# Performance work log

Measured on AMD Instinct MI355X. Metric: run time of the kernel, lower is better.

Reference implementation:

```python
import jax, jax.numpy as jnp
import numpy as np
from math import comb

LEVEL = 16
LENGTH = 64
TOPK = 2
SIZE = 512
BATCH = 32
NEG = -1e8


def _catalan(n_leaves):
    # number of distinct binary trees over n_leaves leaves
    m = n_leaves - 1
    return comb(2 * m, m) // (m + 1)


def _offsets(length, level):
    # cell offset of each chart level: level l occupies (length - l) cells
    return np.cumsum([0] + [length - l for l in range(level)])


def setup_inputs() -> dict:
    key = jax.random.key(0)
    K, B, size, level, length = TOPK, BATCH, SIZE, LEVEL, LENGTH
    L, N = length - level, level
    off = _offsets(length, level)
    ncells = int(off[-1])
    ks = jax.random.split(key, 5)
    chart_h = jax.random.normal(ks[0], (K, B, ncells, size), jnp.float32)
    chart_s = jax.random.normal(ks[1], (K, B, ncells, 1), jnp.float32)
    mat = jax.random.normal(ks[2], (size, size), jnp.float32) / np.sqrt(size).astype(np.float32)
    Wc = jax.random.normal(ks[3], (2 * size, size), jnp.float32) / np.sqrt(2 * size).astype(np.float32)
    bc = jnp.zeros((size,), jnp.float32)
    # structural gather indices: left child = (level n, pos), right child = (level level-1-n, pos+n+1)
    l_idx = np.zeros((L, N), np.int64)
    r_idx = np.zeros((L, N), np.int64)
    for pos in range(L):
        for n in range(N):
            l_idx[pos, n] = off[n] + pos
            r_idx[pos, n] = off[level - 1 - n] + pos + n + 1
    return {
        'chart_h': chart_h, 'chart_s': chart_s,
        'l_index': jnp.asarray(l_idx.reshape(-1)), 'r_index': jnp.asarray(r_idx.reshape(-1)),
        'mat': mat, 'Wc': Wc, 'bc': bc,
    }


def _penalty_mask(level, N, K):
    # Faithful to penalize_incomplete_splits: idx = i // K**2 == 0 for i < K*K,
    # so only the n_idx==0 block is ever penalized. l_level=0, r_level=level-1.
    M = N * K * K
    mask = np.zeros(M, bool)
    for i in range(K * K):
        lk, rk = i // K, i % K
        if _catalan(0 + 1) < lk + 1 or _catalan((level - 1) + 1) < rk + 1:
            mask[i] = True
    return jnp.asarray(mask)


def reference(chart_h, chart_s, l_index, r_index, mat, Wc, bc):
    K, B, ncells, size = chart_h.shape
    level = LEVEL
    N = level
    L = l_index.shape[0] // N
    M = N * K * K
    # gather child states from charts: (K,B,L,N,size) -> (B,L,N,K,size)
    lh = jnp.moveaxis(chart_h[:, :, l_index].reshape(K, B, L, N, size), 0, 3)
    rh = jnp.moveaxis(chart_h[:, :, r_index].reshape(K, B, L, N, size), 0, 3)
    ls = jnp.moveaxis(chart_s[:, :, l_index].reshape(K, B, L, N), 0, 3)  # (B,L,N,K)
    rs = jnp.moveaxis(chart_s[:, :, r_index].reshape(K, B, L, N), 0, 3)
    # bilinear composition score: (B,L,N,K_l,K_r)
    s_raw = jnp.einsum('blnkd,de,blnje->blnkj', lh, mat, rh)
    # flat combo index = n*K*K + lk*K + rk; add child scores
    s = (s_raw + ls[..., :, None] + rs[..., None, :]).reshape(B, L, M)
    s = jnp.where(_penalty_mask(level, N, K), jnp.float32(NEG), s)
    topk_s, topk_idx = jax.lax.top_k(s, K)  # (B,L,K), sorted descending like torch.topk
    # dense compose over all N*K*K combos
    combo_lh = jnp.repeat(lh, K, axis=3).reshape(B, L, M, size)   # lk = z // K
    combo_rh = jnp.tile(rh, (1, 1, 1, K, 1)).reshape(B, L, M, size)  # rk = z % K
    all_h = jnp.tanh(jnp.concatenate([combo_lh, combo_rh], axis=-1) @ Wc + bc)
    topk_h = jnp.take_along_axis(all_h, topk_idx[..., None], axis=2)  # (B,L,K,size)
    # UnitNorm normalize_func
    topk_h = topk_h / jnp.linalg.norm(topk_h, axis=-1, keepdims=True)
    topk_s = topk_s[..., None]  # (B,L,K,1) to match torch shape
    if _catalan(N + 1) < K:  # static no-op at this level
        topk_s = topk_s.at[:, :, _catalan(N + 1):].set(NEG)
    topk_n_idx = topk_idx // (K * K)
    topk_lk = (topk_idx % (K * K)) // K
    topk_rk = (topk_idx % (K * K)) % K
    return topk_h, topk_s, topk_n_idx, topk_lk, topk_rk
```

## Files before the change

kernel.cpp:

```cpp
#include <hip/hip_runtime.h>
#include <cstdint>
#include <cstddef>

#define B_DIM   32
#define L_DIM   48
#define NCELLS  904
#define SZ      512
#define NEGF    (-1e8f)
#define DELTA   0.25f
#define MAXC    32

#define OFF_S   1572864
#define OFF_N   1575936
#define OFF_L   1579008
#define OFF_R   1582080

typedef _Float16  f16x8 __attribute__((ext_vector_type(8)));
typedef float     f32x4 __attribute__((ext_vector_type(4)));

static __device__ __forceinline__ uint16_t f2bf(float f) {
    uint32_t u = __builtin_bit_cast(uint32_t, f);
    u += 0x7fffu + ((u >> 16) & 1u);
    return (uint16_t)(u >> 16);
}

#define GLD16(gp, lp) __builtin_amdgcn_global_load_lds(                        \
        (__attribute__((address_space(1))) void*)(gp),                         \
        (__attribute__((address_space(3))) void*)(lp), 16, 0, 0)

static __device__ __forceinline__ int level_off(int n) {
    return n * 64 - (n * (n - 1)) / 2;
}

__global__ __launch_bounds__(256)
void prep_mat(const float* __restrict__ mat, _Float16* __restrict__ mat16)
{
    const size_t j = ((size_t)blockIdx.x * 256 + threadIdx.x) * 8;
    const float4 c = *(const float4*)(mat + j);
    const float4 d = *(const float4*)(mat + j + 4);
    f16x8 w;
    w[0]=(_Float16)(c.x*64.f); w[1]=(_Float16)(c.y*64.f);
    w[2]=(_Float16)(c.z*64.f); w[3]=(_Float16)(c.w*64.f);
    w[4]=(_Float16)(d.x*64.f); w[5]=(_Float16)(d.y*64.f);
    w[6]=(_Float16)(d.z*64.f); w[7]=(_Float16)(d.w*64.f);
    *(f16x8*)(mat16 + j) = w;
}

__global__ __launch_bounds__(256, 3)
void gemm_fused(const float* __restrict__ A,
                const _Float16* __restrict__ Bm,
                _Float16* __restrict__ C)
{
    __shared__ float    As32[64 * 32];
    __shared__ _Float16 Bs[256 * 32];

    const int t = threadIdx.x;
    const int wave = t >> 6, lane = t & 63;
    const int n0 = blockIdx.x * 256;
    const int m0 = blockIdx.y * 64;
    const int col_l = lane & 15, quad = lane >> 4;

    f32x4 acc[4][4];
#pragma unroll
    for (int i = 0; i < 4; ++i)
#pragma unroll
        for (int j = 0; j < 4; ++j) acc[i][j] = (f32x4){0.f, 0.f, 0.f, 0.f};

    const int arow = lane >> 3;
    const int aswz = ((lane & 7) ^ arow) * 4;
    const int asw_rd = (col_l & 7) << 4;

    for (int ks = 0; ks < 16; ++ks) {
        const int k0 = ks * 32;
        __syncthreads();
#pragma unroll
        for (int i = 0; i < 2; ++i) {
            const int q = wave * 2 + i;
            GLD16(A + (size_t)(m0 + q * 8 + arow) * 512 + k0 + aswz,
                  (char*)As32 + q * 1024);
        }
#pragma unroll
        for (int i = 0; i < 4; ++i) {
            const int q = wave * 4 + i;
            GLD16(Bm + (size_t)(n0 + q * 16 + col_l) * 512 + k0 + quad * 8,
                  (char*)Bs + q * 1024);
        }
        __syncthreads();

        f16x8 af[4];
#pragma unroll
        for (int mi = 0; mi < 4; ++mi) {
            const char* rb = (const char*)As32 + mi * 2048 + col_l * 128;
            const f32x4 p0 = *(const f32x4*)(rb + ((quad * 32 +  0) ^ asw_rd));
            const f32x4 p1 = *(const f32x4*)(rb + ((quad * 32 + 16) ^ asw_rd));
#pragma unroll
            for (int j = 0; j < 4; ++j) {
                af[mi][j]     = (_Float16)(p0[j] * 16.f);
                af[mi][j + 4] = (_Float16)(p1[j] * 16.f);
            }
        }
#pragma unroll
        for (int ni = 0; ni < 4; ++ni) {
            const f16x8 bf = *(const f16x8*)&Bs[(wave * 4 + ni) * 512 + lane * 8];
#pragma unroll
            for (int mi = 0; mi < 4; ++mi)
                acc[mi][ni] = __builtin_amdgcn_mfma_f32_16x16x32_f16(
                    af[mi], bf, acc[mi][ni], 0, 0, 0);
        }
    }

#pragma unroll
    for (int ni = 0; ni < 4; ++ni) {
        const int ncol = n0 + wave * 64 + ni * 16 + col_l;
#pragma unroll
        for (int mi = 0; mi < 4; ++mi) {
            const int mrow = m0 + mi * 16 + quad * 4;
#pragma unroll
            for (int r = 0; r < 4; ++r)
                C[(size_t)(mrow + r) * 512 + ncol] = (_Float16)acc[mi][ni][r];
        }
    }
}

static __device__ __forceinline__ void emit_outputs(
    int row, int i1, int i2, float v1, float v2, float* out)
{
    out[OFF_S + row * 2 + 0] = v1;
    out[OFF_S + row * 2 + 1] = v2;
    out[OFF_N + row * 2 + 0] = (float)(i1 >> 2);
    out[OFF_N + row * 2 + 1] = (float)(i2 >> 2);
    out[OFF_L + row * 2 + 0] = (float)((i1 >> 1) & 1);
    out[OFF_L + row * 2 + 1] = (float)((i2 >> 1) & 1);
    out[OFF_R + row * 2 + 0] = (float)(i1 & 1);
    out[OFF_R + row * 2 + 1] = (float)(i2 & 1);
}

static __device__ __forceinline__ void gather_x(
    int row, int pos, int b, const int* top_z,
    const float* __restrict__ chart_h, uint16_t* __restrict__ X, int tid)
{
#pragma unroll
    for (int kq = 0; kq < 2; ++kq) {
        const int z = top_z[kq];
        const int n = z >> 2, lk = (z >> 1) & 1, rk = z & 1;
        const int lcell = level_off(n) + pos;
        const int rcell = level_off(15 - n) + pos + n + 1;
        const float* srcl = chart_h + ((size_t)(lk * B_DIM + b) * NCELLS + lcell) * SZ;
        const float* srcr = chart_h + ((size_t)(rk * B_DIM + b) * NCELLS + rcell) * SZ;
        uint16_t* dst = X + ((size_t)row * 2 + kq) * 1024;
        const int e = tid * 2;
        const float2 a = *(const float2*)(srcl + e);
        const float2 c = *(const float2*)(srcr + e);
        *(uint32_t*)(dst + e)       = (uint32_t)f2bf(a.x) | ((uint32_t)f2bf(a.y) << 16);
        *(uint32_t*)(dst + 512 + e) = (uint32_t)f2bf(c.x) | ((uint32_t)f2bf(c.y) << 16);
    }
}

__global__ __launch_bounds__(256)
void score_topk(const float* __restrict__ chart_h,
                const _Float16* __restrict__ T16,
                const float* __restrict__ chart_s,
                uint32_t* __restrict__ items,
                int* __restrict__ rowbase,
                int* __restrict__ counter,
                int* __restrict__ flags,
                uint16_t* __restrict__ X,
                float* __restrict__ out)
{
    const int b   = blockIdx.x / L_DIM;
    const int pos = blockIdx.x % L_DIM;
    const int row = blockIdx.x;
    const int wave = threadIdx.x >> 6, lane = threadIdx.x & 63;

    __shared__ float s_sh[64];
    __shared__ int top_z[2];
    __shared__ int flag_sh;

#pragma unroll
    for (int ni = 0; ni < 4; ++ni) {
        const int n = wave * 4 + ni;
        const int lcell = level_off(n) + pos;
        const int rcell = level_off(15 - n) + pos + n + 1;

        const float* lp0 = chart_h + ((size_t)(0 * B_DIM + b) * NCELLS + lcell) * SZ + lane * 8;
        const float* lp1 = chart_h + ((size_t)(1 * B_DIM + b) * NCELLS + lcell) * SZ + lane * 8;
        const float4 l0a = *(const float4*)lp0, l0b = *(const float4*)(lp0 + 4);
        const float4 l1a = *(const float4*)lp1, l1b = *(const float4*)(lp1 + 4);
        const f16x8 t0 = *(const f16x8*)(T16 + ((size_t)(0 * B_DIM + b) * NCELLS + rcell) * SZ + lane * 8);
        const f16x8 t1 = *(const f16x8*)(T16 + ((size_t)(1 * B_DIM + b) * NCELLS + rcell) * SZ + lane * 8);

        float l0[8] = {l0a.x, l0a.y, l0a.z, l0a.w, l0b.x, l0b.y, l0b.z, l0b.w};
        float l1[8] = {l1a.x, l1a.y, l1a.z, l1a.w, l1b.x, l1b.y, l1b.z, l1b.w};

        float d00 = 0.f, d01 = 0.f, d10 = 0.f, d11 = 0.f;
#pragma unroll
        for (int j = 0; j < 8; ++j) {
            const float c0 = (float)t0[j], c1 = (float)t1[j];
            d00 += l0[j] * c0; d01 += l0[j] * c1;
            d10 += l1[j] * c0; d11 += l1[j] * c1;
        }
#pragma unroll
        for (int o = 32; o > 0; o >>= 1) {
            d00 += __shfl_down(d00, o);
            d01 += __shfl_down(d01, o);
            d10 += __shfl_down(d10, o);
            d11 += __shfl_down(d11, o);
        }
        if (lane == 0) {
            const float ls0 = chart_s[(size_t)(0 * B_DIM + b) * NCELLS + lcell];
            const float ls1 = chart_s[(size_t)(1 * B_DIM + b) * NCELLS + lcell];
            const float rs0 = chart_s[(size_t)(0 * B_DIM + b) * NCELLS + rcell];
            const float rs1 = chart_s[(size_t)(1 * B_DIM + b) * NCELLS + rcell];
            const float inv = 1.0f / 1024.0f;
            s_sh[n * 4 + 0] = d00 * inv + ls0 + rs0;
            s_sh[n * 4 + 1] = d01 * inv + ls0 + rs1;
            s_sh[n * 4 + 2] = d10 * inv + ls1 + rs0;
            s_sh[n * 4 + 3] = d11 * inv + ls1 + rs1;
        }
    }
    __syncthreads();

    if (threadIdx.x < 64) {
        float v = s_sh[lane];
        if (lane == 2 || lane == 3) v = NEGF;
        float v1 = v; int i1 = lane;
#pragma unroll
        for (int o = 32; o > 0; o >>= 1) {
            float ov = __shfl_down(v1, o);
            int   oi = __shfl_down(i1, o);
            if (ov > v1 || (ov == v1 && oi < i1)) { v1 = ov; i1 = oi; }
        }
        v1 = __shfl(v1, 0); i1 = __shfl(i1, 0);
        float v2 = (lane == i1) ? -3.4e38f : v; int i2 = lane;
#pragma unroll
        for (int o = 32; o > 0; o >>= 1) {
            float ov = __shfl_down(v2, o);
            int   oi = __shfl_down(i2, o);
            if (ov > v2 || (ov == v2 && oi < i2)) { v2 = ov; i2 = oi; }
        }
        v2 = __shfl(v2, 0); i2 = __shfl(i2, 0);
        float v3 = (lane == i1 || lane == i2) ? -3.4e38f : v;
#pragma unroll
        for (int o = 32; o > 0; o >>= 1) {
            const float ov = __shfl_down(v3, o);
            if (ov > v3) v3 = ov;
        }
        v3 = __shfl(v3, 0);

        const int f = (v1 - v2 < DELTA) || (v2 - v3 < DELTA);
        const bool cand = (v >= v2 - DELTA);
        const unsigned long long mask = __ballot(cand);
        const int nc_full = __popcll(mask);
        const int nc = nc_full < MAXC ? nc_full : MAXC;
        int base = 0;
        if (lane == 0) {
            flags[row] = f ? nc : 0;
            flag_sh = f;
            if (f) base = atomicAdd(counter, nc);
            rowbase[row] = base;
            top_z[0] = i1; top_z[1] = i2;
            if (!f) emit_outputs(row, i1, i2, v1, v2, out);
        }
        base = __shfl(base, 0);
        if (f && cand) {
            const int rank = __popcll(mask & ((1ull << lane) - 1ull));
            if (rank < MAXC) items[base + rank] = ((uint32_t)row << 6) | (uint32_t)lane;
        }
    }
    __syncthreads();

    if (!flag_sh)
        gather_x(row, pos, b, top_z, chart_h, X, threadIdx.x);
}

__global__ __launch_bounds__(256)
void refine_eval(const float* __restrict__ chart_h,
                 const float* __restrict__ chart_s,
                 const float* __restrict__ mat,
                 const uint32_t* __restrict__ items,
                 const int* __restrict__ counter,
                 float* __restrict__ exval)
{
    const int total = *counter;
    const int t = threadIdx.x;
    const int wave = t >> 6, lane = t & 63;

    __shared__ float lh_sh[2][512];
    __shared__ float psum[2][4];

    for (int p = blockIdx.x; 2 * p < total; p += gridDim.x) {
        const int it0 = 2 * p;
        const int it1v = (2 * p + 1 < total);
        const uint32_t item0 = items[it0];
        const uint32_t item1 = it1v ? items[it0 + 1] : item0;

        int rowA = item0 >> 6, zA = item0 & 63;
        int bA = rowA / L_DIM, posA = rowA % L_DIM;
        int nA = zA >> 2, lkA = (zA >> 1) & 1, rkA = zA & 1;
        int lcA = level_off(nA) + posA, rcA = level_off(15 - nA) + posA + nA + 1;
        int rowB = item1 >> 6, zB = item1 & 63;
        int bB = rowB / L_DIM, posB = rowB % L_DIM;
        int nB = zB >> 2, lkB = (zB >> 1) & 1, rkB = zB & 1;
        int lcB = level_off(nB) + posB, rcB = level_off(15 - nB) + posB + nB + 1;

        const float* lhA = chart_h + ((size_t)(lkA * B_DIM + bA) * NCELLS + lcA) * SZ;
        const float* rhA = chart_h + ((size_t)(rkA * B_DIM + bA) * NCELLS + rcA) * SZ;
        const float* lhB = chart_h + ((size_t)(lkB * B_DIM + bB) * NCELLS + lcB) * SZ;
        const float* rhB = chart_h + ((size_t)(rkB * B_DIM + bB) * NCELLS + rcB) * SZ;

        __syncthreads();
        lh_sh[0][t] = lhA[t]; lh_sh[0][t + 256] = lhA[t + 256];
        lh_sh[1][t] = lhB[t]; lh_sh[1][t + 256] = lhB[t + 256];
        const float4 rA0 = *(const float4*)(rhA + lane * 8);
        const float4 rA1 = *(const float4*)(rhA + lane * 8 + 4);
        const float4 rB0 = *(const float4*)(rhB + lane * 8);
        const float4 rB1 = *(const float4*)(rhB + lane * 8 + 4);
        __syncthreads();

        const float* mb = mat + (size_t)(wave * 128) * 512 + lane * 8;
        float a00 = 0.f, a01 = 0.f, b00 = 0.f, b01 = 0.f;
        for (int e = 0; e < 128; e += 2) {
            const float4 m0 = *(const float4*)(mb + (size_t)(e + 0) * 512);
            const float4 m1 = *(const float4*)(mb + (size_t)(e + 0) * 512 + 4);
            const float4 m2 = *(const float4*)(mb + (size_t)(e + 1) * 512);
            const float4 m3 = *(const float4*)(mb + (size_t)(e + 1) * 512 + 4);
            const int eg = wave * 128 + e;
            const float lA0 = lh_sh[0][eg],     lB0 = lh_sh[1][eg];
            const float lA1 = lh_sh[0][eg + 1], lB1 = lh_sh[1][eg + 1];
            const float dA0 = m0.x*rA0.x + m0.y*rA0.y + m0.z*rA0.z + m0.w*rA0.w
                            + m1.x*rA1.x + m1.y*rA1.y + m1.z*rA1.z + m1.w*rA1.w;
            const float dB0 = m0.x*rB0.x + m0.y*rB0.y + m0.z*rB0.z + m0.w*rB0.w
                            + m1.x*rB1.x + m1.y*rB1.y + m1.z*rB1.z + m1.w*rB1.w;
            const float dA1 = m2.x*rA0.x + m2.y*rA0.y + m2.z*rA0.z + m2.w*rA0.w
                            + m3.x*rA1.x + m3.y*rA1.y + m3.z*rA1.z + m3.w*rA1.w;
            const float dB1 = m2.x*rB0.x + m2.y*rB0.y + m2.z*rB0.z + m2.w*rB0.w
                            + m3.x*rB1.x + m3.y*rB1.y + m3.z*rB1.z + m3.w*rB1.w;
            a00 += lA0 * dA0; a01 += lA1 * dA1;
            b00 += lB0 * dB0; b01 += lB1 * dB1;
        }
        float sA = a00 + a01, sB = b00 + b01;
#pragma unroll
        for (int o = 32; o > 0; o >>= 1) {
            sA += __shfl_down(sA, o);
            sB += __shfl_down(sB, o);
        }
        if (lane == 0) { psum[0][wave] = sA; psum[1][wave] = sB; }
        __syncthreads();
        if (t == 0) {
            const float lsA = chart_s[(size_t)(lkA * B_DIM + bA) * NCELLS + lcA];
            const float rsA = chart_s[(size_t)(rkA * B_DIM + bA) * NCELLS + rcA];
            exval[it0] = psum[0][0] + psum[0][1] + psum[0][2] + psum[0][3] + lsA + rsA;
            if (it1v) {
                const float lsB = chart_s[(size_t)(lkB * B_DIM + bB) * NCELLS + lcB];
                const float rsB = chart_s[(size_t)(rkB * B_DIM + bB) * NCELLS + rcB];
                exval[it0 + 1] = psum[1][0] + psum[1][1] + psum[1][2] + psum[1][3] + lsB + rsB;
            }
        }
    }
}

__global__ __launch_bounds__(256)
void refine_pick(const float* __restrict__ chart_h,
                 const uint32_t* __restrict__ items,
                 const int* __restrict__ rowbase,
                 const int* __restrict__ flags,
                 const float* __restrict__ exval,
                 uint16_t* __restrict__ X,
                 float* __restrict__ out)
{
    const int row = blockIdx.x;
    const int nc = flags[row];
    if (nc == 0) return;
    const int b = row / L_DIM, pos = row % L_DIM;
    const int t = threadIdx.x;

    __shared__ int top_z[2];

    if (t == 0) {
        const int base = rowbase[row];
        float v1 = -3.4e38f; int c1 = -1;
        for (int c = 0; c < nc; ++c) {
            const float v = exval[base + c];
            if (v > v1) { v1 = v; c1 = c; }
        }
        float v2 = -3.4e38f; int c2 = -1;
        for (int c = 0; c < nc; ++c) {
            if (c == c1) continue;
            const float v = exval[base + c];
            if (v > v2) { v2 = v; c2 = c; }
        }
        const int i1 = (int)(items[base + c1] & 63u);
        const int i2 = (int)(items[base + c2] & 63u);
        top_z[0] = i1; top_z[1] = i2;
        emit_outputs(row, i1, i2, v1, v2, out);
    }
    __syncthreads();
    gather_x(row, pos, b, top_z, chart_h, X, t);
}

__global__ __launch_bounds__(256)
void transpose_wc(const float* __restrict__ Wc, uint16_t* __restrict__ WcT)
{
    __shared__ float tbuf[64][65];
    const int i0 = blockIdx.x * 64;
    const int o0 = blockIdx.y * 64;
    const int c = threadIdx.x & 63, r4 = threadIdx.x >> 6;
    for (int rr = r4; rr < 64; rr += 4)
        tbuf[rr][c] = Wc[(size_t)(i0 + rr) * 512 + o0 + c];
    __syncthreads();
    for (int rr = r4; rr < 64; rr += 4)
        WcT[(size_t)(o0 + rr) * 1024 + i0 + c] = f2bf(tbuf[c][rr]);
}

typedef __bf16 bf16x8 __attribute__((ext_vector_type(8)));

__global__ __launch_bounds__(256, 2)
void gemm_compose(const uint16_t* __restrict__ A,
                  const uint16_t* __restrict__ Bm,
                  const float* __restrict__ bias,
                  float* __restrict__ C,
                  int M, int Nn, int Kk)
{
    __shared__ uint16_t As[128 * 64];
    __shared__ uint16_t Bs[128 * 64];

    const int tid  = threadIdx.x;
    const int wave = tid >> 6, lane = tid & 63;
    const int m0 = blockIdx.x * 128, n0 = blockIdx.y * 128;
    const int wm = (wave & 1) * 64, wn = (wave >> 1) * 64;
    const int col_l = lane & 15, quad = lane >> 4;
    const int lrow = lane >> 3;
    const int lcol = (lane & 7) * 8;

    f32x4 acc[4][4];
#pragma unroll
    for (int i = 0; i < 4; ++i)
#pragma unroll
        for (int j = 0; j < 4; ++j) acc[i][j] = (f32x4){0.f, 0.f, 0.f, 0.f};

    for (int k0 = 0; k0 < Kk; k0 += 64) {
        __syncthreads();
#pragma unroll
        for (int i = 0; i < 4; ++i) {
            const int q = wave * 4 + i;
            const int r = q * 8 + lrow;
            GLD16(A  + (size_t)(m0 + r) * Kk + k0 + lcol, (char*)As + q * 1024);
            GLD16(Bm + (size_t)(n0 + r) * Kk + k0 + lcol, (char*)Bs + q * 1024);
        }
        __syncthreads();
#pragma unroll
        for (int kk = 0; kk < 64; kk += 32) {
            bf16x8 af[4], bfr[4];
#pragma unroll
            for (int mi = 0; mi < 4; ++mi)
                af[mi] = *(const bf16x8*)&As[(wm + mi * 16 + col_l) * 64 + kk + quad * 8];
#pragma unroll
            for (int ni = 0; ni < 4; ++ni)
                bfr[ni] = *(const bf16x8*)&Bs[(wn + ni * 16 + col_l) * 64 + kk + quad * 8];
#pragma unroll
            for (int mi = 0; mi < 4; ++mi)
#pragma unroll
                for (int ni = 0; ni < 4; ++ni)
                    acc[mi][ni] = __builtin_amdgcn_mfma_f32_16x16x32_bf16(
                        af[mi], bfr[ni], acc[mi][ni], 0, 0, 0);
        }
    }

#pragma unroll
    for (int ni = 0; ni < 4; ++ni) {
        const int ncol = n0 + wn + ni * 16 + col_l;
        const float bv = bias[ncol];
#pragma unroll
        for (int mi = 0; mi < 4; ++mi) {
            const int mrow = m0 + wm + mi * 16 + quad * 4;
#pragma unroll
            for (int r = 0; r < 4; ++r)
                C[(size_t)(mrow + r) * Nn + ncol] = tanhf(acc[mi][ni][r] + bv);
        }
    }
}

__global__ __launch_bounds__(256)
void norm_rows(const float* __restrict__ H, float* __restrict__ out)
{
    const int row = blockIdx.x;
    const float* h = H + (size_t)row * SZ;
    const int t = threadIdx.x;
    const int wave = t >> 6, lane = t & 63;
    const float a = h[t], c = h[t + 256];
    float ss = a * a + c * c;
#pragma unroll
    for (int o = 32; o > 0; o >>= 1) ss += __shfl_down(ss, o);
    __shared__ float wsum[4];
    if (lane == 0) wsum[wave] = ss;
    __syncthreads();
    const float inv = rsqrtf(wsum[0] + wsum[1] + wsum[2] + wsum[3]);
    out[(size_t)row * SZ + t]       = a * inv;
    out[(size_t)row * SZ + t + 256] = c * inv;
}

extern "C" void kernel_launch(void* const* d_in, const int* in_sizes, int n_in,
                              void* d_out, int out_size, void* d_ws, size_t ws_size,
                              hipStream_t stream)
{
    const float* chart_h = (const float*)d_in[0];
    const float* chart_s = (const float*)d_in[1];
    const float* mat = (const float*)d_in[4];
    const float* Wc  = (const float*)d_in[5];
    const float* bc  = (const float*)d_in[6];
    float* out = (float*)d_out;

    char* ws = (char*)d_ws;
    _Float16* T16   = (_Float16*)ws;
    _Float16* MAT16 = (_Float16*)(ws + 59244544);
    uint32_t* ITEMS = (uint32_t*)(ws + 59768832);
    float*    EXVAL = (float*)(ws + 59965440);
    int*      RBASE = (int*)(ws + 60162048);
    int*      CNT   = (int*)(ws + 60168192);
    int*      FLAGS = (int*)(ws + 60168448);
    uint16_t* X     = (uint16_t*)(ws + 60174592);
    uint16_t* WcT   = (uint16_t*)ws;
    float*    H     = (float*)(ws + 1048576);

    hipMemsetAsync(CNT, 0, 4, stream);
    prep_mat<<<dim3(128), 256, 0, stream>>>(mat, MAT16);
    gemm_fused<<<dim3(2, 904), 256, 0, stream>>>(chart_h, MAT16, T16);
    score_topk<<<dim3(B_DIM * L_DIM), 256, 0, stream>>>(chart_h, T16, chart_s,
                                                        ITEMS, RBASE, CNT, FLAGS, X, out);
    transpose_wc<<<dim3(16, 8), 256, 0, stream>>>(Wc, WcT);
    refine_eval<<<dim3(1024), 256, 0, stream>>>(chart_h, chart_s, mat, ITEMS, CNT, EXVAL);
    refine_pick<<<dim3(B_DIM * L_DIM), 256, 0, stream>>>(chart_h, ITEMS, RBASE, FLAGS,
                                                         EXVAL, X, out);
    gemm_compose<<<dim3(24, 4), 256, 0, stream>>>(X, WcT, bc, H, 3072, 512, 1024);
    norm_rows<<<dim3(3072), 256, 0, stream>>>(H, out);
}
```

Baseline: 341.4 us.

## Pre-pack mat into MFMA fragment layout and double the GEMM K-step

prep_mat now writes the fp16 weight matrix pre-arranged into 16x32 MFMA fragment chunks, so each B tile is loaded into LDS as contiguous 1KB blocks. The GEMM K loop drops from 16 iterations of 32 to 8 iterations of 64, which halves the barriers. A tiles are loaded through registers, converted to fp16 once and stored in LDS in fragment order instead of as fp32 with swizzled reads. The K-step start is staggered by blockIdx.y to spread concurrent blocks across memory. LDS use grows, which could lower occupancy under launch_bounds(256,3).

```diff
diff --git a/kernel.cpp b/kernel.cpp
--- a/kernel.cpp
+++ b/kernel.cpp
@@ -33,32 +33,37 @@
 }
 
 __global__ __launch_bounds__(256)
-void prep_mat(const float* __restrict__ mat, _Float16* __restrict__ mat16)
-{
-    const size_t j = ((size_t)blockIdx.x * 256 + threadIdx.x) * 8;
-    const float4 c = *(const float4*)(mat + j);
-    const float4 d = *(const float4*)(mat + j + 4);
+void prep_mat(const float* __restrict__ mat, _Float16* __restrict__ P)
+{
+    const int tg   = blockIdx.x * 256 + threadIdx.x;
+    const int c    = tg >> 6, lane = tg & 63;
+    const int srow = 16 * (c & 31) + (lane & 15);
+    const int scol = 32 * (c >> 5) + (lane >> 4) * 8;
+    const float4 a = *(const float4*)(mat + (size_t)srow * 512 + scol);
+    const float4 b = *(const float4*)(mat + (size_t)srow * 512 + scol + 4);
     f16x8 w;
-    w[0]=(_Float16)(c.x*64.f); w[1]=(_Float16)(c.y*64.f);
-    w[2]=(_Float16)(c.z*64.f); w[3]=(_Float16)(c.w*64.f);
-    w[4]=(_Float16)(d.x*64.f); w[5]=(_Float16)(d.y*64.f);
-    w[6]=(_Float16)(d.z*64.f); w[7]=(_Float16)(d.w*64.f);
-    *(f16x8*)(mat16 + j) = w;
+    w[0]=(_Float16)(a.x*64.f); w[1]=(_Float16)(a.y*64.f);
+    w[2]=(_Float16)(a.z*64.f); w[3]=(_Float16)(a.w*64.f);
+    w[4]=(_Float16)(b.x*64.f); w[5]=(_Float16)(b.y*64.f);
+    w[6]=(_Float16)(b.z*64.f); w[7]=(_Float16)(b.w*64.f);
+    *(f16x8*)(P + (size_t)tg * 8) = w;
 }
 
 __global__ __launch_bounds__(256, 3)
 void gemm_fused(const float* __restrict__ A,
-                const _Float16* __restrict__ Bm,
+                const _Float16* __restrict__ P,
                 _Float16* __restrict__ C)
 {
-    __shared__ float    As32[64 * 32];
-    __shared__ _Float16 Bs[256 * 32];
+    __shared__ _Float16 As16[8 * 512];
+    __shared__ _Float16 Bs[32 * 512];
 
     const int t = threadIdx.x;
     const int wave = t >> 6, lane = t & 63;
     const int n0 = blockIdx.x * 256;
+    const int nq = n0 >> 4;
     const int m0 = blockIdx.y * 64;
     const int col_l = lane & 15, quad = lane >> 4;
+    const int stag = blockIdx.y & 7;
 
     f32x4 acc[4][4];
 #pragma unroll
@@ -66,46 +71,53 @@
 #pragma unroll
         for (int j = 0; j < 4; ++j) acc[i][j] = (f32x4){0.f, 0.f, 0.f, 0.f};
 
-    const int arow = lane >> 3;
-    const int aswz = ((lane & 7) ^ arow) * 4;
-    const int asw_rd = (col_l & 7) << 4;
-
-    for (int ks = 0; ks < 16; ++ks) {
-        const int k0 = ks * 32;
-        __syncthreads();
-#pragma unroll
-        for (int i = 0; i < 2; ++i) {
-            const int q = wave * 2 + i;
-            GLD16(A + (size_t)(m0 + q * 8 + arow) * 512 + k0 + aswz,
-                  (char*)As32 + q * 1024);
-        }
-#pragma unroll
-        for (int i = 0; i < 4; ++i) {
-            const int q = wave * 4 + i;
-            GLD16(Bm + (size_t)(n0 + q * 16 + col_l) * 512 + k0 + quad * 8,
-                  (char*)Bs + q * 1024);
-        }
-        __syncthreads();
-
-        f16x8 af[4];
-#pragma unroll
-        for (int mi = 0; mi < 4; ++mi) {
-            const char* rb = (const char*)As32 + mi * 2048 + col_l * 128;
-            const f32x4 p0 = *(const f32x4*)(rb + ((quad * 32 +  0) ^ asw_rd));
-            const f32x4 p1 = *(const f32x4*)(rb + ((quad * 32 + 16) ^ asw_rd));
+    for (int ks = 0; ks < 8; ++ks) {
+        const int kse = (ks + stag) & 7;
+        __syncthreads();
+
+        f32x4 p0[2], p1[2];
+#pragma unroll
+        for (int h = 0; h < 2; ++h) {
+            const int c  = wave * 2 + h;
+            const int kki = c >> 2, mi = c & 3;
+            const float* ap = A + (size_t)(m0 + mi * 16 + col_l) * 512
+                                + kse * 64 + kki * 32 + quad * 8;
+            p0[h] = *(const f32x4*)ap;
+            p1[h] = *(const f32x4*)(ap + 4);
+        }
+#pragma unroll
+        for (int i2 = 0; i2 < 8; ++i2) {
+            const int idx = wave * 8 + i2;
+            const int kki = idx >> 4, i = idx & 15;
+            const int c = (kse * 2 + kki) * 32 + nq + i;
+            GLD16(P + (size_t)c * 512 + lane * 8, (char*)Bs + idx * 1024);
+        }
+#pragma unroll
+        for (int h = 0; h < 2; ++h) {
+            f16x8 av;
 #pragma unroll
             for (int j = 0; j < 4; ++j) {
-                af[mi][j]     = (_Float16)(p0[j] * 16.f);
-                af[mi][j + 4] = (_Float16)(p1[j] * 16.f);
+                av[j]     = (_Float16)(p0[h][j] * 16.f);
+                av[j + 4] = (_Float16)(p1[h][j] * 16.f);
             }
-        }
-#pragma unroll
-        for (int ni = 0; ni < 4; ++ni) {
-            const f16x8 bf = *(const f16x8*)&Bs[(wave * 4 + ni) * 512 + lane * 8];
+            *(f16x8*)&As16[(wave * 2 + h) * 512 + lane * 8] = av;
+        }
+        __syncthreads();
+
+#pragma unroll
+        for (int kki = 0; kki < 2; ++kki) {
+            f16x8 af[4];
 #pragma unroll
             for (int mi = 0; mi < 4; ++mi)
-                acc[mi][ni] = __builtin_amdgcn_mfma_f32_16x16x32_f16(
-                    af[mi], bf, acc[mi][ni], 0, 0, 0);
+                af[mi] = *(const f16x8*)&As16[(kki * 4 + mi) * 512 + lane * 8];
+#pragma unroll
+            for (int ni = 0; ni < 4; ++ni) {
+                const f16x8 bf = *(const f16x8*)&Bs[(kki * 16 + wave * 4 + ni) * 512 + lane * 8];
+#pragma unroll
+                for (int mi = 0; mi < 4; ++mi)
+                    acc[mi][ni] = __builtin_amdgcn_mfma_f32_16x16x32_f16(
+                        af[mi], bf, acc[mi][ni], 0, 0, 0);
+            }
         }
     }
 
```

Result: faster. 315.4 us (-7.6%).
